# Kernel tuning notes

Measured on AMD Instinct MI355X. Metric: run time of the kernel, lower is better.

The kernel has to match this reference:

```python
import jax, jax.numpy as jnp
import numpy as np

D = 1024      # emb_dim
H = 16        # nb_heads
HD = D // H   # head_dim
DFF = 4096    # d_ffn
V = 32000     # vocab_size
T = 1024      # context_size
L = 6         # nb_layers
N_POS = 10000


def _uinit(key, shape, scale):
    # init_tensor: uniform(-1,1) / sqrt(size[scale_dim])
    return (2.0 * jax.random.uniform(key, shape, dtype=jnp.float32) - 1.0) / np.sqrt(scale).astype(np.float32)


def setup_inputs() -> dict:
    key = jax.random.key(0)
    ks = jax.random.split(key, 18)
    # one-hot token input (1, t, u)
    tok = jax.random.randint(ks[0], (T,), 0, V)
    X = jax.nn.one_hot(tok, V, dtype=jnp.float32)[None]
    W_emb = _uinit(ks[1], (V, D), V)
    # sinusoidal positional embedding, interleaved sin/cos columns
    r = np.float32(N_POS ** (-2.0 / D))
    t = jnp.arange(T, dtype=jnp.float32)
    kk = jnp.arange(D // 2, dtype=jnp.float32)
    theta = t[:, None] * (r ** kk)[None, :]              # (t, d/2)
    pos = jnp.stack([jnp.sin(theta), jnp.cos(theta)], axis=2).reshape(T, D)
    WQ = _uinit(ks[2], (L, H, D, HD), D)
    WK = _uinit(ks[3], (L, H, D, HD), D)
    WV = _uinit(ks[4], (L, H, D, HD), D)
    Wout = _uinit(ks[5], (L, D, D), D)
    ln1_g = _uinit(ks[6], (L, D), D)
    ln1_b = _uinit(ks[7], (L, D), D)
    ln2_g = _uinit(ks[8], (L, D), D)
    ln2_b = _uinit(ks[9], (L, D), D)
    w1 = _uinit(ks[10], (L, DFF, D), D)   # torch Linear weight (out,in)
    b1 = _uinit(ks[11], (L, DFF), D)
    w2 = _uinit(ks[12], (L, D, DFF), DFF)
    b2 = _uinit(ks[13], (L, D), DFF)
    last_g = _uinit(ks[14], (D,), D)
    last_b = _uinit(ks[15], (D,), D)
    return dict(X=X, W_emb=W_emb, pos=pos, WQ=WQ, WK=WK, WV=WV, Wout=Wout,
                ln1_g=ln1_g, ln1_b=ln1_b, ln2_g=ln2_g, ln2_b=ln2_b,
                w1=w1, b1=b1, w2=w2, b2=b2, last_g=last_g, last_b=last_b)


def _layernorm(Y, g, b):
    # NOTE: normalizes over the SEQUENCE axis (dim=1 of (1,t,d)), unbiased std (ddof=1),
    # matching the original torch code exactly.
    mu = jnp.mean(Y, axis=1, keepdims=True)
    sd = jnp.std(Y, axis=1, keepdims=True, ddof=1)
    return b + g * (Y - mu) / sd


def _mhsa(Y, wq, wk, wv, wo):
    # Y: (1,t,d); wq/wk/wv: (n,d,h); wo: (d,d)
    Q = jnp.einsum('btd,ndh->nth', Y, wq)
    K = jnp.einsum('btd,ndh->nth', Y, wk)
    Vv = jnp.einsum('btd,ndh->nth', Y, wv)
    Z = jnp.einsum('nth,nsh->nts', Q, K) / jnp.sqrt(jnp.float32(HD))
    A = jax.nn.softmax(Z, axis=-1)
    R = jnp.einsum('nts,nsh->nth', A, Vv)               # (n,t,h)
    Xo = jnp.transpose(R, (1, 0, 2)).reshape(T, D)       # (t,d)
    return Xo @ wo                                        # (t,d); broadcasts back to (1,t,d)


def reference(X, W_emb, pos, WQ, WK, WV, Wout, ln1_g, ln1_b, ln2_g, ln2_b,
              w1, b1, w2, b2, last_g, last_b):
    Xe = jnp.matmul(X, W_emb) + pos                       # (1,t,d)
    for l in range(L):
        Y = Xe + _mhsa(_layernorm(Xe, ln1_g[l], ln1_b[l]), WQ[l], WK[l], WV[l], Wout[l])
        h = jax.nn.relu(jnp.einsum('btd,fd->btf', _layernorm(Y, ln2_g[l], ln2_b[l]), w1[l]) + b1[l])
        Xe = Y + jnp.einsum('btf,df->btd', h, w2[l]) + b2[l]
    return _layernorm(Xe, last_g, last_b)
```

## Files before the change

kernel.cpp:

```cpp
#include <hip/hip_runtime.h>


#define TD   1024
#define DD   1024
#define NH   16
#define HDIM 64
#define FF   4096
#define VOC  32000
#define NL   6

typedef __bf16 bf16;
typedef __bf16 bf16x4 __attribute__((ext_vector_type(4)));
typedef __bf16 bf16x8 __attribute__((ext_vector_type(8)));
typedef float  f32x4  __attribute__((ext_vector_type(4)));

__device__ __forceinline__ void gload_lds16(const void* g, void* l) {
  __builtin_amdgcn_global_load_lds(
      (__attribute__((address_space(1))) void*)(g),
      (__attribute__((address_space(3))) void*)(l), 16, 0, 0);
}

__global__ __launch_bounds__(256) void embed_kernel(
    const float* __restrict__ X, const float* __restrict__ Wemb,
    const float* __restrict__ pos, float* __restrict__ Xe)
{
  const int t = blockIdx.x;
  __shared__ int sidx;
  const float4* row = (const float4*)(X + (size_t)t * VOC);
  for (int i = threadIdx.x; i < VOC / 4; i += 256) {
    float4 v = row[i];
    if (v.x > 0.5f) sidx = 4 * i;
    if (v.y > 0.5f) sidx = 4 * i + 1;
    if (v.z > 0.5f) sidx = 4 * i + 2;
    if (v.w > 0.5f) sidx = 4 * i + 3;
  }
  __syncthreads();
  const float4* w = (const float4*)(Wemb + (size_t)sidx * DD);
  const float4* p = (const float4*)(pos + (size_t)t * DD);
  float4* o = (float4*)(Xe + (size_t)t * DD);
  const int d = threadIdx.x;
  float4 a = w[d], b = p[d];
  o[d] = make_float4(a.x + b.x, a.y + b.y, a.z + b.z, a.w + b.w);
}

__global__ __launch_bounds__(256) void ln_stats_kernel(
    const float* __restrict__ Y, float* __restrict__ part)
{
  const int col = blockIdx.x * 256 + threadIdx.x;
  const int tc  = blockIdx.y;
  const float* p = Y + (size_t)(tc * 32) * DD + col;
  float s = 0.f, s2 = 0.f;
  #pragma unroll 8
  for (int t = 0; t < 32; ++t) {
    float v = p[(size_t)t * DD];
    s += v;
    s2 = fmaf(v, v, s2);
  }
  part[col * 64 + tc]      = s;
  part[col * 64 + 32 + tc] = s2;
}

template<typename OutT>
__global__ __launch_bounds__(256) void ln_apply_kernel(
    const float* __restrict__ Y, const float* __restrict__ part,
    const float* __restrict__ g, const float* __restrict__ b,
    OutT* __restrict__ out)
{
  const int col = blockIdx.x * 256 + threadIdx.x;
  const int tc  = blockIdx.y;
  float s = 0.f, s2 = 0.f;
  const float* pp = part + col * 64;
  #pragma unroll
  for (int i = 0; i < 32; ++i) { s += pp[i]; s2 += pp[32 + i]; }
  const float mu  = s * (1.0f / TD);
  const float var = (s2 - (float)TD * mu * mu) * (1.0f / (TD - 1));
  const float inv = 1.0f / sqrtf(var);
  const float gi  = g[col] * inv;
  const float bb  = b[col];
  const float* yp = Y   + (size_t)(tc * 32) * DD + col;
  OutT*        op = out + (size_t)(tc * 32) * DD + col;
  #pragma unroll 8
  for (int t = 0; t < 32; ++t)
    op[(size_t)t * DD] = (OutT)fmaf(gi, yp[(size_t)t * DD] - mu, bb);
}

template<typename ST>
__global__ __launch_bounds__(256) void transpose_cast(
    const ST* __restrict__ src, int lds_, long long sZ,
    bf16* __restrict__ dst, int ldd, long long dZ)
{
  __shared__ ST tile[64][65];
  src += (size_t)blockIdx.z * sZ + (size_t)(blockIdx.x * 64) * lds_ + blockIdx.y * 64;
  dst += (size_t)blockIdx.z * dZ + (size_t)(blockIdx.y * 64) * ldd + blockIdx.x * 64;
  const int tid = threadIdx.x;
  #pragma unroll
  for (int k = 0; k < 16; ++k) {
    const int idx = tid + k * 256;
    const int r = idx >> 6, c = idx & 63;
    tile[r][c] = src[(size_t)r * lds_ + c];
  }
  __syncthreads();
  #pragma unroll
  for (int k = 0; k < 16; ++k) {
    const int idx = tid + k * 256;
    const int r = idx >> 6, c = idx & 63;
    dst[(size_t)r * ldd + c] = (bf16)(float)tile[c][r];
  }
}

__global__ __launch_bounds__(256) void cast_bf4(
    const float* __restrict__ s, bf16* __restrict__ d, int n4)
{
  const int i = blockIdx.x * 256 + threadIdx.x;
  if (i < n4) {
    float4 v = ((const float4*)s)[i];
    bf16x4 o = { (bf16)v.x, (bf16)v.y, (bf16)v.z, (bf16)v.w };
    ((bf16x4*)d)[i] = o;
  }
}

template<int BM, int BN, int WGM, int WGN, bool OUTBF, bool BIAS, bool RESID, bool RELU>
__global__ __launch_bounds__(256) void gemm_bf16(
    const bf16* __restrict__ A, const bf16* __restrict__ B,
    const float* __restrict__ bias, const float* __restrict__ R,
    void* __restrict__ Cv,
    int K, int lda, int ldb, int ldc,
    long long sA, long long sB, long long sC, float alpha)
{
  constexpr int FM = BM / WGM / 16;
  constexpr int FN = BN / WGN / 16;
  __shared__ bf16 sm[(BM + BN) * 64];
  bf16* As = sm;
  bf16* Bs = sm + BM * 64;

  const int z = blockIdx.z;
  A += (size_t)z * sA + (size_t)(blockIdx.x * BM) * lda;
  B += (size_t)z * sB + (size_t)(blockIdx.y * BN) * ldb;

  const int tid  = threadIdx.x;
  const int lane = tid & 63;
  const int wv   = tid >> 6;
  const int lr   = lane >> 3;
  const int lk   = (lane & 7) * 8;
  const int wr   = (wv / WGN) * FM * 16;
  const int wc   = (wv % WGN) * FN * 16;
  const int l15  = lane & 15;
  const int l16  = lane >> 4;

  f32x4 acc[FM][FN] = {};

  for (int k0 = 0; k0 < K; k0 += 64) {
    #pragma unroll
    for (int s8 = 0; s8 < BM / 32; ++s8) {
      const int s = s8 * 4 + wv;
      gload_lds16(A + (size_t)(s * 8 + lr) * lda + (k0 + lk), As + s * 512);
    }
    #pragma unroll
    for (int s8 = 0; s8 < BN / 32; ++s8) {
      const int s = s8 * 4 + wv;
      gload_lds16(B + (size_t)(s * 8 + lr) * ldb + (k0 + lk), Bs + s * 512);
    }
    __syncthreads();

    #pragma unroll
    for (int ks = 0; ks < 2; ++ks) {
      const int ko = ks * 32 + l16 * 8;
      bf16x8 af[FM], bg[FN];
      #pragma unroll
      for (int i = 0; i < FM; ++i)
        af[i] = *(const bf16x8*)(As + (wr + i * 16 + l15) * 64 + ko);
      #pragma unroll
      for (int j = 0; j < FN; ++j)
        bg[j] = *(const bf16x8*)(Bs + (wc + j * 16 + l15) * 64 + ko);
      #pragma unroll
      for (int i = 0; i < FM; ++i)
        #pragma unroll
        for (int j = 0; j < FN; ++j)
          acc[i][j] = __builtin_amdgcn_mfma_f32_16x16x32_bf16(af[i], bg[j], acc[i][j], 0, 0, 0);
    }
    __syncthreads();
  }

  const int brow = blockIdx.x * BM;
  const int bcol = blockIdx.y * BN;
  float* Cf = (float*)Cv;
  bf16*  Cb = (bf16*)Cv;
  #pragma unroll
  for (int i = 0; i < FM; ++i) {
    const int r0 = brow + wr + i * 16 + l16 * 4;
    #pragma unroll
    for (int j = 0; j < FN; ++j) {
      const int c = bcol + wc + j * 16 + l15;
      float bsv = 0.f;
      if constexpr (BIAS) bsv = bias[c];
      #pragma unroll
      for (int r = 0; r < 4; ++r) {
        float v = acc[i][j][r] * alpha + bsv;
        if constexpr (RESID) v += R[(size_t)(r0 + r) * ldc + c];
        if constexpr (RELU)  v = fmaxf(v, 0.f);
        const size_t off = (size_t)z * sC + (size_t)(r0 + r) * ldc + c;
        if constexpr (OUTBF) Cb[off] = (bf16)v; else Cf[off] = v;
      }
    }
  }
}

__global__ __launch_bounds__(256) void flash_attn(
    const bf16* __restrict__ QKV, const bf16* __restrict__ Vt,
    bf16* __restrict__ XO)
{
  const int h   = blockIdx.y;
  const int t0  = blockIdx.x * 64;
  const int tid = threadIdx.x;
  const int lane = tid & 63;
  const int wv  = tid >> 6;
  const int l15 = lane & 15, l16 = lane >> 4;
  const int lr  = lane >> 3, lk = (lane & 7) * 8;

  __shared__ bf16 Ks[128 * 64];
  __shared__ bf16 Vs[64 * 128];
  __shared__ bf16 Ps[64 * 128];

  bf16x8 qf[2];
  #pragma unroll
  for (int ks = 0; ks < 2; ++ks)
    qf[ks] = *(const bf16x8*)(QKV + (size_t)(t0 + wv * 16 + l15) * 3072
                              + h * 64 + ks * 32 + l16 * 8);

  f32x4 o[4] = {};
  float m[4], lsum[4];
  #pragma unroll
  for (int r = 0; r < 4; ++r) { m[r] = -1e30f; lsum[r] = 0.f; }

  for (int kv = 0; kv < TD; kv += 128) {
    #pragma unroll
    for (int i = 0; i < 4; ++i) {
      const int sr = i * 4 + wv;
      gload_lds16(QKV + (size_t)(kv + sr * 8 + lr) * 3072 + 1024 + h * 64 + lk,
                  Ks + sr * 512);
    }
    #pragma unroll
    for (int i = 0; i < 4; ++i) {
      const int sr = i * 4 + wv;
      gload_lds16(Vt + (size_t)(h * 64 + sr * 4 + l16) * 1024 + kv + l15 * 8,
                  Vs + sr * 512);
    }
    __syncthreads();

    f32x4 st[8] = {};
    #pragma unroll
    for (int ks = 0; ks < 2; ++ks) {
      #pragma unroll
      for (int j = 0; j < 8; ++j) {
        bf16x8 kf = *(const bf16x8*)(Ks + (j * 16 + l15) * 64 + ks * 32 + l16 * 8);
        st[j] = __builtin_amdgcn_mfma_f32_16x16x32_bf16(qf[ks], kf, st[j], 0, 0, 0);
      }
    }

    #pragma unroll
    for (int r = 0; r < 4; ++r) {
      float mx = -1e30f;
      #pragma unroll
      for (int j = 0; j < 8; ++j) { st[j][r] *= 0.125f; mx = fmaxf(mx, st[j][r]); }
      #pragma unroll
      for (int off = 8; off; off >>= 1) mx = fmaxf(mx, __shfl_xor(mx, off, 64));
      const float nm = fmaxf(m[r], mx);
      const float sc = __expf(m[r] - nm);
      m[r] = nm;
      const int row = wv * 16 + l16 * 4 + r;
      char* prow = (char*)Ps + row * 256;
      float rs = 0.f;
      #pragma unroll
      for (int j = 0; j < 8; ++j) {
        float p = __expf(st[j][r] - nm);
        rs += p;
        *(bf16*)(prow + ((((j * 16 + l15) * 2)) ^ ((row & 7) << 4))) = (bf16)p;
      }
      #pragma unroll
      for (int off = 8; off; off >>= 1) rs += __shfl_xor(rs, off, 64);
      lsum[r] = lsum[r] * sc + rs;
      #pragma unroll
      for (int jo = 0; jo < 4; ++jo) o[jo][r] *= sc;
    }
    __syncthreads();

    const int arow = wv * 16 + l15;
    #pragma unroll
    for (int ks2 = 0; ks2 < 4; ++ks2) {
      bf16x8 pa = *(const bf16x8*)((char*)Ps + arow * 256 +
                     ((ks2 * 64 + l16 * 16) ^ ((arow & 7) << 4)));
      #pragma unroll
      for (int jo = 0; jo < 4; ++jo) {
        bf16x8 vf = *(const bf16x8*)(Vs + (jo * 16 + l15) * 128 + ks2 * 32 + l16 * 8);
        o[jo] = __builtin_amdgcn_mfma_f32_16x16x32_bf16(pa, vf, o[jo], 0, 0, 0);
      }
    }
    __syncthreads();
  }

  #pragma unroll
  for (int r = 0; r < 4; ++r) {
    const float rinv = 1.0f / lsum[r];
    const int row = t0 + wv * 16 + l16 * 4 + r;
    #pragma unroll
    for (int jo = 0; jo < 4; ++jo)
      XO[(size_t)row * DD + h * 64 + jo * 16 + l15] = (bf16)(o[jo][r] * rinv);
  }
}

extern "C" void kernel_launch(void* const* d_in, const int* in_sizes, int n_in,
                              void* d_out, int out_size, void* d_ws, size_t ws_size,
                              hipStream_t stream)
{
  const float* X     = (const float*)d_in[0];
  const float* Wemb  = (const float*)d_in[1];
  const float* pos   = (const float*)d_in[2];
  const float* WQ    = (const float*)d_in[3];
  const float* WK    = (const float*)d_in[4];
  const float* WV    = (const float*)d_in[5];
  const float* Wout  = (const float*)d_in[6];
  const float* ln1g  = (const float*)d_in[7];
  const float* ln1b  = (const float*)d_in[8];
  const float* ln2g  = (const float*)d_in[9];
  const float* ln2b  = (const float*)d_in[10];
  const float* w1    = (const float*)d_in[11];
  const float* b1    = (const float*)d_in[12];
  const float* w2    = (const float*)d_in[13];
  const float* b2    = (const float*)d_in[14];
  const float* lastg = (const float*)d_in[15];
  const float* lastb = (const float*)d_in[16];
  float* out = (float*)d_out;

  char* w = (char*)d_ws;
  float* XE    = (float*)(w + 0);
  float* Yb    = (float*)(w + 4194304);
  float* part  = (float*)(w + 8388608);
  bf16*  LNbf  = (bf16*)(w + 8650752);
  bf16*  QKVb  = (bf16*)(w + 10747904);
  bf16*  Vt    = (bf16*)(w + 17039360);
  bf16*  XO    = (bf16*)(w + 19136512);
  bf16*  Hb    = (bf16*)(w + 21233664);
  bf16*  QwAll = (bf16*)(w + 29622272);
  bf16*  KwAll = (bf16*)(w + 42205184);
  bf16*  VwAll = (bf16*)(w + 54788096);
  bf16*  WoAll = (bf16*)(w + 67371008);
  bf16*  w1b   = (bf16*)(w + 79953920);
  bf16*  w2b   = (bf16*)(w + 88342528);

  transpose_cast<float><<<dim3(16, 1, NL * NH), 256, 0, stream>>>(
      WQ, HDIM, (long long)DD * HDIM, QwAll, DD, (long long)HDIM * DD);
  transpose_cast<float><<<dim3(16, 1, NL * NH), 256, 0, stream>>>(
      WK, HDIM, (long long)DD * HDIM, KwAll, DD, (long long)HDIM * DD);
  transpose_cast<float><<<dim3(16, 1, NL * NH), 256, 0, stream>>>(
      WV, HDIM, (long long)DD * HDIM, VwAll, DD, (long long)HDIM * DD);
  transpose_cast<float><<<dim3(16, 16, NL), 256, 0, stream>>>(
      Wout, DD, (long long)DD * DD, WoAll, DD, (long long)DD * DD);

  embed_kernel<<<TD, 256, 0, stream>>>(X, Wemb, pos, XE);

  for (int l = 0; l < NL; ++l) {
    const float* b1l = b1 + (size_t)l * FF;
    const float* b2l = b2 + (size_t)l * DD;

    cast_bf4<<<FF * DD / 4 / 256, 256, 0, stream>>>(w1 + (size_t)l * FF * DD, w1b, FF * DD / 4);
    cast_bf4<<<FF * DD / 4 / 256, 256, 0, stream>>>(w2 + (size_t)l * DD * FF, w2b, FF * DD / 4);

    ln_stats_kernel<<<dim3(4, 32), 256, 0, stream>>>(XE, part);
    ln_apply_kernel<bf16><<<dim3(4, 32), 256, 0, stream>>>(
        XE, part, ln1g + l * DD, ln1b + l * DD, LNbf);

    gemm_bf16<64, 128, 2, 2, true, false, false, false><<<dim3(16, 8, 3), 256, 0, stream>>>(
        LNbf, QwAll + (size_t)l * DD * DD, nullptr, nullptr, QKVb,
        DD, DD, DD, 3 * DD, 0LL, 6LL * 1024 * 1024, 1024LL, 1.0f);

    transpose_cast<bf16><<<dim3(16, 16, 1), 256, 0, stream>>>(
        QKVb + 2048, 3 * DD, 0LL, Vt, TD, 0LL);

    flash_attn<<<dim3(TD / 64, NH), 256, 0, stream>>>(QKVb, Vt, XO);

    gemm_bf16<64, 64, 2, 2, false, false, true, false><<<dim3(16, 16, 1), 256, 0, stream>>>(
        XO, WoAll + (size_t)l * DD * DD, nullptr, XE, Yb,
        DD, DD, DD, DD, 0LL, 0LL, 0LL, 1.0f);

    ln_stats_kernel<<<dim3(4, 32), 256, 0, stream>>>(Yb, part);
    ln_apply_kernel<bf16><<<dim3(4, 32), 256, 0, stream>>>(
        Yb, part, ln2g + l * DD, ln2b + l * DD, LNbf);

    gemm_bf16<64, 128, 2, 2, true, true, false, true><<<dim3(16, 32, 1), 256, 0, stream>>>(
        LNbf, w1b, b1l, nullptr, Hb, DD, DD, DD, FF, 0LL, 0LL, 0LL, 1.0f);

    gemm_bf16<64, 64, 2, 2, false, true, true, false><<<dim3(16, 16, 1), 256, 0, stream>>>(
        Hb, w2b, b2l, Yb, XE, FF, FF, FF, DD, 0LL, 0LL, 0LL, 1.0f);
  }

  ln_stats_kernel<<<dim3(4, 32), 256, 0, stream>>>(XE, part);
  ln_apply_kernel<float><<<dim3(4, 32), 256, 0, stream>>>(XE, part, lastg, lastb, out);
}
```

Before: 1.465 ms.

## Split-K output GEMMs with fused residual+stats reduce, bigger tiles, hoist weight casts

Moves the Wout and w2 GEMMs to 128x128 tiles with a 4-way split-K into an fp32 scratch buffer. A new reduce kernel sums the partials and adds residual and bias, and it also produces the layernorm statistics, so the separate stats kernels go away. The QKV and w1 GEMMs move to 128x128 tiles. When the workspace is large enough, all layers' FFN weights are cast to bf16 once up front instead of per layer. The cost is extra fp32 partial-sum traffic and a larger workspace.

```diff
diff --git a/kernel.cpp b/kernel.cpp
--- a/kernel.cpp
+++ b/kernel.cpp
@@ -82,6 +82,30 @@
   #pragma unroll 8
   for (int t = 0; t < 32; ++t)
     op[(size_t)t * DD] = (OutT)fmaf(gi, yp[(size_t)t * DD] - mu, bb);
+}
+
+template<bool BIAS>
+__global__ __launch_bounds__(256) void reduce4_stats(
+    const float* __restrict__ SK, const float* __restrict__ bias,
+    const float* __restrict__ resid, float* __restrict__ out,
+    float* __restrict__ part)
+{
+  const int col = blockIdx.x * 256 + threadIdx.x;
+  const int tc  = blockIdx.y;
+  const float bb = BIAS ? bias[col] : 0.f;
+  float s = 0.f, s2 = 0.f;
+  #pragma unroll 4
+  for (int t = 0; t < 32; ++t) {
+    const size_t idx = (size_t)(tc * 32 + t) * DD + col;
+    float v = resid[idx] + bb
+            + SK[idx] + SK[idx + (size_t)TD * DD]
+            + SK[idx + 2 * (size_t)TD * DD] + SK[idx + 3 * (size_t)TD * DD];
+    out[idx] = v;
+    s += v;
+    s2 = fmaf(v, v, s2);
+  }
+  part[col * 64 + tc]      = s;
+  part[col * 64 + 32 + tc] = s2;
 }
 
 template<typename ST>
@@ -340,12 +364,14 @@
   bf16*  Vt    = (bf16*)(w + 17039360);
   bf16*  XO    = (bf16*)(w + 19136512);
   bf16*  Hb    = (bf16*)(w + 21233664);
-  bf16*  QwAll = (bf16*)(w + 29622272);
-  bf16*  KwAll = (bf16*)(w + 42205184);
-  bf16*  VwAll = (bf16*)(w + 54788096);
-  bf16*  WoAll = (bf16*)(w + 67371008);
-  bf16*  w1b   = (bf16*)(w + 79953920);
-  bf16*  w2b   = (bf16*)(w + 88342528);
+  float* SK    = (float*)(w + 29622272);
+  bf16*  QwAll = (bf16*)(w + 46399488);
+  bf16*  KwAll = (bf16*)(w + 58982400);
+  bf16*  VwAll = (bf16*)(w + 71565312);
+  bf16*  WoAll = (bf16*)(w + 84148224);
+  const bool allW = ws_size >= 195428352ULL;
+  bf16* w1b = (bf16*)(w + 96731136);
+  bf16* w2b = allW ? (bf16*)(w + 147062784) : (bf16*)(w + 105119744);
 
   transpose_cast<float><<<dim3(16, 1, NL * NH), 256, 0, stream>>>(
       WQ, HDIM, (long long)DD * HDIM, QwAll, DD, (long long)HDIM * DD);
@@ -355,21 +381,28 @@
       WV, HDIM, (long long)DD * HDIM, VwAll, DD, (long long)HDIM * DD);
   transpose_cast<float><<<dim3(16, 16, NL), 256, 0, stream>>>(
       Wout, DD, (long long)DD * DD, WoAll, DD, (long long)DD * DD);
+  if (allW) {
+    cast_bf4<<<NL * FF * DD / 4 / 256, 256, 0, stream>>>(w1, w1b, NL * FF * DD / 4);
+    cast_bf4<<<NL * FF * DD / 4 / 256, 256, 0, stream>>>(w2, w2b, NL * FF * DD / 4);
+  }
 
   embed_kernel<<<TD, 256, 0, stream>>>(X, Wemb, pos, XE);
+  ln_stats_kernel<<<dim3(4, 32), 256, 0, stream>>>(XE, part);
 
   for (int l = 0; l < NL; ++l) {
     const float* b1l = b1 + (size_t)l * FF;
     const float* b2l = b2 + (size_t)l * DD;
-
-    cast_bf4<<<FF * DD / 4 / 256, 256, 0, stream>>>(w1 + (size_t)l * FF * DD, w1b, FF * DD / 4);
-    cast_bf4<<<FF * DD / 4 / 256, 256, 0, stream>>>(w2 + (size_t)l * DD * FF, w2b, FF * DD / 4);
-
-    ln_stats_kernel<<<dim3(4, 32), 256, 0, stream>>>(XE, part);
+    bf16* w1bl = allW ? w1b + (size_t)l * FF * DD : w1b;
+    bf16* w2bl = allW ? w2b + (size_t)l * DD * FF : w2b;
+    if (!allW) {
+      cast_bf4<<<FF * DD / 4 / 256, 256, 0, stream>>>(w1 + (size_t)l * FF * DD, w1bl, FF * DD / 4);
+      cast_bf4<<<FF * DD / 4 / 256, 256, 0, stream>>>(w2 + (size_t)l * DD * FF, w2bl, FF * DD / 4);
+    }
+
     ln_apply_kernel<bf16><<<dim3(4, 32), 256, 0, stream>>>(
         XE, part, ln1g + l * DD, ln1b + l * DD, LNbf);
 
-    gemm_bf16<64, 128, 2, 2, true, false, false, false><<<dim3(16, 8, 3), 256, 0, stream>>>(
+    gemm_bf16<128, 128, 2, 2, true, false, false, false><<<dim3(8, 8, 3), 256, 0, stream>>>(
         LNbf, QwAll + (size_t)l * DD * DD, nullptr, nullptr, QKVb,
         DD, DD, DD, 3 * DD, 0LL, 6LL * 1024 * 1024, 1024LL, 1.0f);
 
@@ -378,21 +411,22 @@
 
     flash_attn<<<dim3(TD / 64, NH), 256, 0, stream>>>(QKVb, Vt, XO);
 
-    gemm_bf16<64, 64, 2, 2, false, false, true, false><<<dim3(16, 16, 1), 256, 0, stream>>>(
-        XO, WoAll + (size_t)l * DD * DD, nullptr, XE, Yb,
-        DD, DD, DD, DD, 0LL, 0LL, 0LL, 1.0f);
-
-    ln_stats_kernel<<<dim3(4, 32), 256, 0, stream>>>(Yb, part);
+    gemm_bf16<128, 128, 2, 2, false, false, false, false><<<dim3(8, 8, 4), 256, 0, stream>>>(
+        XO, WoAll + (size_t)l * DD * DD, nullptr, nullptr, SK,
+        256, DD, DD, DD, 256LL, 256LL, (long long)TD * DD, 1.0f);
+    reduce4_stats<false><<<dim3(4, 32), 256, 0, stream>>>(SK, nullptr, XE, Yb, part);
+
     ln_apply_kernel<bf16><<<dim3(4, 32), 256, 0, stream>>>(
         Yb, part, ln2g + l * DD, ln2b + l * DD, LNbf);
 
-    gemm_bf16<64, 128, 2, 2, true, true, false, true><<<dim3(16, 32, 1), 256, 0, stream>>>(
-        LNbf, w1b, b1l, nullptr, Hb, DD, DD, DD, FF, 0LL, 0LL, 0LL, 1.0f);
-
-    gemm_bf16<64, 64, 2, 2, false, true, true, false><<<dim3(16, 16, 1), 256, 0, stream>>>(
-        Hb, w2b, b2l, Yb, XE, FF, FF, FF, DD, 0LL, 0LL, 0LL, 1.0f);
-  }
-
-  ln_stats_kernel<<<dim3(4, 32), 256, 0, stream>>>(XE, part);
+    gemm_bf16<128, 128, 2, 2, true, true, false, true><<<dim3(8, 32, 1), 256, 0, stream>>>(
+        LNbf, w1bl, b1l, nullptr, Hb, DD, DD, DD, FF, 0LL, 0LL, 0LL, 1.0f);
+
+    gemm_bf16<128, 128, 2, 2, false, false, false, false><<<dim3(8, 8, 4), 256, 0, stream>>>(
+        Hb, w2bl, nullptr, nullptr, SK,
+        1024, FF, FF, DD, 1024LL, 1024LL, (long long)TD * DD, 1.0f);
+    reduce4_stats<true><<<dim3(4, 32), 256, 0, stream>>>(SK, b2l, Yb, XE, part);
+  }
+
   ln_apply_kernel<float><<<dim3(4, 32), 256, 0, stream>>>(XE, part, lastg, lastb, out);
 }
```

Measured after the change: 1.417 ms. 3.3% less time.
